# Kernel optimization log

Hardware: AMD Instinct MI355X
Metric: run time of the kernel (lower is better)

The kernel has to match this reference:

```python
import jax, jax.numpy as jnp
import numpy as np

B, S, D, H = 1, 2048, 4096, 32
HD = D // H  # 128


def setup_inputs() -> dict:
    key = jax.random.key(0)
    ks = jax.random.split(key, 6)
    x = jax.random.normal(ks[0], (B, S, D), dtype=jnp.float32)
    # rotary angles: standard llama freqs, position * inv_freq
    inv_freq = 1.0 / (10000.0 ** (jnp.arange(0, HD, 2, dtype=jnp.float32) / HD))  # (HD/2,)
    freqs = jnp.arange(S, dtype=jnp.float32)[:, None] * inv_freq[None, :]  # (S, HD/2)
    scale = 0.02
    wq = jax.random.normal(ks[1], (D, D), dtype=jnp.float32) * scale
    wk = jax.random.normal(ks[2], (D, D), dtype=jnp.float32) * scale
    wv = jax.random.normal(ks[3], (D, D), dtype=jnp.float32) * scale
    wo = jax.random.normal(ks[4], (D, D), dtype=jnp.float32) * scale
    return {"x": x, "freqs": freqs, "wq": wq, "wk": wk, "wv": wv, "wo": wo}


def _rope(t, cos, sin):
    # t: (B,S,H,HD); pairs are interleaved (complex view of last dim)
    b, s, h, d = t.shape
    t2 = t.reshape(b, s, h, d // 2, 2)
    t0, t1 = t2[..., 0], t2[..., 1]
    o0 = t0 * cos - t1 * sin
    o1 = t0 * sin + t1 * cos
    return jnp.stack([o0, o1], axis=-1).reshape(b, s, h, d)


def reference(x, freqs, wq, wk, wv, wo):
    b, s, d = x.shape
    hd = 2 * freqs.shape[-1]
    h = d // hd
    # projections (torch Linear: y = x @ W.T)
    q = (x @ wq.T).reshape(b, s, h, hd)
    k = (x @ wk.T).reshape(b, s, h, hd)
    v = (x @ wv.T).reshape(b, s, h, hd)
    cos = jnp.cos(freqs)[None, :s, None, :]  # (1,S,1,HD/2)
    sin = jnp.sin(freqs)[None, :s, None, :]
    q = _rope(q, cos, sin)
    k = _rope(k, cos, sin)
    q = q.transpose(0, 2, 1, 3)  # (B,H,S,HD)
    k = k.transpose(0, 2, 1, 3)
    v = v.transpose(0, 2, 1, 3)
    scale = jnp.sqrt(jnp.float32(hd))
    scores = jnp.einsum('bhqd,bhkd->bhqk', q, k).astype(jnp.float32) / scale
    # causal mask (qp == ep path): -inf strictly above diagonal
    mask = jnp.triu(jnp.full((s, s), -jnp.inf, dtype=scores.dtype), k=1)
    scores = scores + mask[None, None]
    attn = jax.nn.softmax(scores, axis=-1).astype(q.dtype)
    out = jnp.einsum('bhqk,bhkd->bhqd', attn, v)
    out = out.transpose(0, 2, 1, 3).reshape(b, s, d)
    return out @ wo.T
```

## Files before the change

kernel.cpp:

```cpp
#include <hip/hip_runtime.h>
#include <hip/hip_bf16.h>
#include <stdint.h>


typedef __attribute__((ext_vector_type(8))) short bf16x8;
typedef __attribute__((ext_vector_type(4))) float f32x4;

#define S_LEN 2048
#define DMODEL 4096
#define NHEAD 32
#define HDIM 128
#define QKV_LD 12288

#define QSCALE 0.1275247584969759f

__device__ __forceinline__ unsigned short f2bf(float f) {
  unsigned int u = __float_as_uint(f);
  unsigned int r = u + 0x7FFFu + ((u >> 16) & 1u);
  return (unsigned short)(r >> 16);
}
__device__ __forceinline__ float bf2f(unsigned short h) {
  return __uint_as_float(((unsigned int)h) << 16);
}
__device__ __forceinline__ void gl_lds16(const void* g, void* l) {
  __builtin_amdgcn_global_load_lds((const __attribute__((address_space(1))) unsigned int*)g,
                                   (__attribute__((address_space(3))) unsigned int*)l, 16, 0, 0);
}
__device__ __forceinline__ void phase_barrier() {
  __builtin_amdgcn_sched_barrier(0);
  asm volatile("" ::: "memory");
  __builtin_amdgcn_s_barrier();
  asm volatile("" ::: "memory");
  __builtin_amdgcn_sched_barrier(0);
}
__device__ __forceinline__ void wait_vmcnt6() {
  __builtin_amdgcn_sched_barrier(0);
  asm volatile("s_waitcnt vmcnt(6)" ::: "memory");
  __builtin_amdgcn_sched_barrier(0);
}
__device__ __forceinline__ void wait_vmcnt4() {
  __builtin_amdgcn_sched_barrier(0);
  asm volatile("s_waitcnt vmcnt(4)" ::: "memory");
  __builtin_amdgcn_sched_barrier(0);
}

__device__ __forceinline__ void cvt4(const float* __restrict__ s, unsigned short* __restrict__ d,
                                     int i) {
  float4 v = ((const float4*)s)[i];
  ushort4 o;
  o.x = f2bf(v.x); o.y = f2bf(v.y); o.z = f2bf(v.z); o.w = f2bf(v.w);
  ((ushort4*)d)[i] = o;
}

__global__ __launch_bounds__(256) void prep_inputs(const float* __restrict__ x,
                                                   const float* __restrict__ wq,
                                                   const float* __restrict__ wk,
                                                   const float* __restrict__ wv,
                                                   const float* __restrict__ fr,
                                                   unsigned short* __restrict__ xb,
                                                   unsigned short* __restrict__ wqkvb,
                                                   float* __restrict__ cs) {
  const int NX = 2097152;
  const int NW = 4194304;
  const int NR = S_LEN * 64;
  const int total = NX + 3 * NW + NR;
  int i = blockIdx.x * blockDim.x + threadIdx.x;
  int stride = gridDim.x * blockDim.x;
  for (; i < total; i += stride) {
    if (i < NX) {
      cvt4(x, xb, i);
    } else if (i < NX + NW) {
      cvt4(wq, wqkvb, i - NX);
    } else if (i < NX + 2 * NW) {
      cvt4(wk, wqkvb + 16777216, i - NX - NW);
    } else if (i < NX + 3 * NW) {
      cvt4(wv, wqkvb + 33554432, i - NX - 2 * NW);
    } else {
      int j = i - (NX + 3 * NW);
      float f = fr[j];
      cs[2 * j]     = cosf(f);
      cs[2 * j + 1] = sinf(f);
    }
  }
}

__device__ __forceinline__ void mfma_quad(f32x4 (&acc)[8][4], const bf16x8 (&af)[4][2],
                                          const bf16x8 (&bf)[2][2], int moff, int noff) {
  __builtin_amdgcn_s_setprio(1);
#pragma unroll
  for (int mi = 0; mi < 4; ++mi)
#pragma unroll
    for (int ni = 0; ni < 2; ++ni)
#pragma unroll
      for (int kk = 0; kk < 2; ++kk)
        acc[moff + mi][noff + ni] = __builtin_amdgcn_mfma_f32_16x16x32_bf16(
            af[mi][kk], bf[ni][kk], acc[moff + mi][noff + ni], 0, 0, 0);
  __builtin_amdgcn_s_setprio(0);
}
__device__ __forceinline__ void mfma_quad2(f32x4 (&acc)[4][4], const bf16x8 (&af)[2][2],
                                           const bf16x8 (&bf)[2][2], int moff, int noff) {
  __builtin_amdgcn_s_setprio(1);
#pragma unroll
  for (int mi = 0; mi < 2; ++mi)
#pragma unroll
    for (int ni = 0; ni < 2; ++ni)
#pragma unroll
      for (int kk = 0; kk < 2; ++kk)
        acc[moff + mi][noff + ni] = __builtin_amdgcn_mfma_f32_16x16x32_bf16(
            af[mi][kk], bf[ni][kk], acc[moff + mi][noff + ni], 0, 0, 0);
  __builtin_amdgcn_s_setprio(0);
}

__device__ __forceinline__ void read_a(bf16x8 (&dst)[4][2], const char* base, int half,
                                       int wr, int l15, int l4, int swz) {
#pragma unroll
  for (int mi = 0; mi < 4; ++mi) {
    const char* rb = base + (wr * 128 + half * 64 + mi * 16 + l15) * 128;
#pragma unroll
    for (int kk = 0; kk < 2; ++kk)
      dst[mi][kk] = *(const bf16x8*)(rb + ((kk * 64 + l4 * 16) ^ swz));
  }
}
__device__ __forceinline__ void read_b(bf16x8 (&dst)[2][2], const char* base, int half,
                                       int wc, int l15, int l4, int swz) {
#pragma unroll
  for (int ni = 0; ni < 2; ++ni) {
    const char* rb = base + (wc * 64 + half * 32 + ni * 16 + l15) * 128;
#pragma unroll
    for (int kk = 0; kk < 2; ++kk)
      dst[ni][kk] = *(const bf16x8*)(rb + ((kk * 64 + l4 * 16) ^ swz));
  }
}
__device__ __forceinline__ void read_a2(bf16x8 (&dst)[2][2], const char* base, int half,
                                        int wr, int l15, int l4, int swz) {
#pragma unroll
  for (int mi = 0; mi < 2; ++mi) {
    const char* rb = base + (wr * 64 + half * 32 + mi * 16 + l15) * 128;
#pragma unroll
    for (int kk = 0; kk < 2; ++kk)
      dst[mi][kk] = *(const bf16x8*)(rb + ((kk * 64 + l4 * 16) ^ swz));
  }
}
__device__ __forceinline__ void read_b2(bf16x8 (&dst)[2][2], const char* base, int half,
                                        int wc, int l15, int l4, int swz) {
#pragma unroll
  for (int ni = 0; ni < 2; ++ni) {
    const char* rb = base + (wc * 64 + half * 32 + ni * 16 + l15) * 128;
#pragma unroll
    for (int kk = 0; kk < 2; ++kk)
      dst[ni][kk] = *(const bf16x8*)(rb + ((kk * 64 + l4 * 16) ^ swz));
  }
}

template <bool OUT_BF16, bool ROPE>
__device__ __forceinline__ void gemm256_body(const unsigned short* __restrict__ A,
                                             const unsigned short* __restrict__ B,
                                             void* __restrict__ C,
                                             int M, int N, int K, int ldc,
                                             char* smem, int wg,
                                             const float* __restrict__ cs) {
  const int tid = threadIdx.x;
  const int lane = tid & 63, wid = tid >> 6;
  const int wr = wid >> 2, wc = wid & 3;
  const int l15 = lane & 15, l4 = lane >> 4;

  const int nbn = N >> 8;
  const int bm = wg / nbn, bn = wg % nbn;
  const int nk = K >> 6;

  unsigned short* AlB = (unsigned short*)smem;
  unsigned short* BlB = (unsigned short*)smem + 32768;

  const int srow = tid >> 3;
  const int scol = ((tid & 7) ^ (srow & 7)) * 8;
  const unsigned short* Asrc = A + (size_t)(bm * 256 + srow) * K + scol;
  const unsigned short* Bsrc = B + (size_t)(bn * 256 + srow) * K + scol;
  const int ldsdst = wid * 512;

#define STA(b, kt, q) gl_lds16(Asrc + ((size_t)(q) * 64) * K + (kt) * 64, AlB + (b) * 16384 + (q) * 4096 + ldsdst)
#define STB(b, kt, q) gl_lds16(Bsrc + ((size_t)(q) * 64) * K + (kt) * 64, BlB + (b) * 16384 + (q) * 4096 + ldsdst)

  const int swz = (l15 & 7) << 4;

  f32x4 acc[8][4] = {};
  bf16x8 Ax[4][2], Ay[4][2], B0f[2][2], B1f[2][2];

#pragma unroll
  for (int q = 0; q < 4; ++q) STA(0, 0, q);
#pragma unroll
  for (int q = 0; q < 4; ++q) STB(0, 0, q);
  {
    const int k1 = (nk > 1) ? 1 : 0;
    STA(1, k1, 0); STA(1, k1, 2);
    STB(1, k1, 0); STB(1, k1, 1); STB(1, k1, 2); STB(1, k1, 3);
  }
  wait_vmcnt6();
  phase_barrier();
  read_a(Ax, (const char*)AlB, 0, wr, l15, l4, swz);
  read_b(B0f, (const char*)BlB, 0, wc, l15, l4, swz);

#define HALF(bb, AC, AA, t)                                                \
  {                                                                        \
    const int kt1 = ((t) + 1 < nk) ? (t) + 1 : nk - 1;                     \
    const int kt2 = ((t) + 2 < nk) ? (t) + 2 : nk - 1;                     \
    const char* Ab = (const char*)(AlB + (bb) * 16384);                    \
    const char* Bb = (const char*)(BlB + (bb) * 16384);                    \
    const char* Abn = (const char*)(AlB + ((bb) ^ 1) * 16384);             \
    const char* Bbn = (const char*)(BlB + ((bb) ^ 1) * 16384);             \
    STA((bb) ^ 1, kt1, 1); STA((bb) ^ 1, kt1, 3);                          \
    phase_barrier();                                                       \
    mfma_quad(acc, AC, B0f, 0, 0);                                 \
    read_a(AA, Ab, 1, wr, l15, l4, swz);                                   \
    STA(bb, kt2, 0); STA(bb, kt2, 2);                                      \
    phase_barrier();                                                       \
    mfma_quad(acc, AA, B0f, 4, 0);                                 \
    read_b(B1f, Bb, 1, wc, l15, l4, swz);                                  \
    STB(bb, kt2, 0); STB(bb, kt2, 1);                                      \
    phase_barrier();                                                       \
    mfma_quad(acc, AA, B1f, 4, 2);                                 \
    STB(bb, kt2, 2); STB(bb, kt2, 3);                                      \
    wait_vmcnt6();                                                         \
    phase_barrier();                                                       \
    mfma_quad(acc, AC, B1f, 0, 2);                                 \
    read_a(AA, Abn, 0, wr, l15, l4, swz);                                  \
    read_b(B0f, Bbn, 0, wc, l15, l4, swz);                                 \
  }

  for (int t = 0; t < nk; t += 2) {
    HALF(0, Ax, Ay, t);
    HALF(1, Ay, Ax, t + 1);
  }
#undef HALF
#undef STA
#undef STB

  __builtin_amdgcn_sched_barrier(0);
  asm volatile("s_waitcnt vmcnt(0)" ::: "memory");

  const size_t crow0 = (size_t)bm * 256 + wr * 128 + l4 * 4;
  const int ccol0 = bn * 256 + wc * 64 + l15;
#pragma unroll
  for (int mf = 0; mf < 8; ++mf)
#pragma unroll
    for (int nf = 0; nf < 4; ++nf) {
      size_t row = crow0 + mf * 16;
      int col = ccol0 + nf * 16;
      if (ROPE) {
        const int d = col & (HDIM - 1);
        const int i2 = d & ~1;
        const float fs = (col < 4096) ? QSCALE : 1.0f;
        unsigned short* Cp = (unsigned short*)C;
#pragma unroll
        for (int r = 0; r < 4; ++r) {
          float v = acc[mf][nf][r];
          float vp = __shfl_xor(v, 1, 64);
          float2 csv = *(const float2*)&cs[(row + r) * HDIM + i2];
          float o = ((d & 1) == 0) ? (v * csv.x - vp * csv.y)
                                   : (vp * csv.y + v * csv.x);
          Cp[(row + r) * ldc + col] = f2bf(o * fs);
        }
      } else if (OUT_BF16) {
        unsigned short* Cp = (unsigned short*)C;
#pragma unroll
        for (int r = 0; r < 4; ++r) Cp[(row + r) * ldc + col] = f2bf(acc[mf][nf][r]);
      } else {
        float* Cp = (float*)C;
#pragma unroll
        for (int r = 0; r < 4; ++r) Cp[(row + r) * ldc + col] = acc[mf][nf][r];
      }
    }
}

template <bool OUT_BF16, bool VT_OUT>
__device__ __forceinline__ void gemm128_body(const unsigned short* __restrict__ A,
                                             const unsigned short* __restrict__ B,
                                             void* __restrict__ C,
                                             int M, int N, int K, int ldc,
                                             char* smem, int wg) {
  const int tid = threadIdx.x;
  const int lane = tid & 63, wid = tid >> 6;
  const int wr = wid >> 2, wc = wid & 3;
  const int l15 = lane & 15, l4 = lane >> 4;

  const int nbn = N >> 8;
  const int bm = wg / nbn, bn = wg % nbn;
  const int nk = K >> 6;

  unsigned short* AlB = (unsigned short*)smem;
  unsigned short* BlB = (unsigned short*)smem + 16384;

  const int srow = tid >> 3;
  const int scol = ((tid & 7) ^ (srow & 7)) * 8;
  const unsigned short* Asrc = A + (size_t)(bm * 128 + srow) * K + scol;
  const unsigned short* Bsrc = B + (size_t)(bn * 256 + srow) * K + scol;
  const int ldsdst = wid * 512;

#define STA2(b, kt, q) gl_lds16(Asrc + ((size_t)(q) * 64) * K + (kt) * 64, AlB + (b) * 8192 + (q) * 4096 + ldsdst)
#define STB2(b, kt, q) gl_lds16(Bsrc + ((size_t)(q) * 64) * K + (kt) * 64, BlB + (b) * 16384 + (q) * 4096 + ldsdst)

  const int swz = (l15 & 7) << 4;

  f32x4 acc[4][4] = {};
  bf16x8 Ax[2][2], Ay[2][2], B0f[2][2], B1f[2][2];

  STA2(0, 0, 0); STA2(0, 0, 1);
#pragma unroll
  for (int q = 0; q < 4; ++q) STB2(0, 0, q);
  {
    const int k1 = (nk > 1) ? 1 : 0;
    STA2(1, k1, 0); STA2(1, k1, 1);
    STB2(1, k1, 0); STB2(1, k1, 1);
  }
  wait_vmcnt4();
  phase_barrier();
  read_a2(Ax, (const char*)AlB, 0, wr, l15, l4, swz);
  read_b2(B0f, (const char*)BlB, 0, wc, l15, l4, swz);

#define HALF2(bb, AC, AA, t)                                               \
  {                                                                        \
    const int kt1 = ((t) + 1 < nk) ? (t) + 1 : nk - 1;                     \
    const int kt2 = ((t) + 2 < nk) ? (t) + 2 : nk - 1;                     \
    const char* Ab = (const char*)(AlB + (bb) * 8192);                     \
    const char* Bb = (const char*)(BlB + (bb) * 16384);                    \
    const char* Abn = (const char*)(AlB + ((bb) ^ 1) * 8192);              \
    const char* Bbn = (const char*)(BlB + ((bb) ^ 1) * 16384);             \
    STB2((bb) ^ 1, kt1, 2); STB2((bb) ^ 1, kt1, 3);        \
    phase_barrier();                                                       \
    mfma_quad2(acc, AC, B0f, 0, 0);                                \
    read_a2(AA, Ab, 1, wr, l15, l4, swz);                                  \
    STA2(bb, kt2, 0); STA2(bb, kt2, 1);                                    \
    phase_barrier();                                                       \
    mfma_quad2(acc, AA, B0f, 2, 0);                                \
    read_b2(B1f, Bb, 1, wc, l15, l4, swz);                                 \
    STB2(bb, kt2, 0); STB2(bb, kt2, 1);                                    \
    phase_barrier();                                                       \
    mfma_quad2(acc, AA, B1f, 2, 2);                                \
    wait_vmcnt4();                                                         \
    phase_barrier();                                                       \
    mfma_quad2(acc, AC, B1f, 0, 2);                                \
    read_a2(AA, Abn, 0, wr, l15, l4, swz);                                 \
    read_b2(B0f, Bbn, 0, wc, l15, l4, swz);                                \
  }

  for (int t = 0; t < nk; t += 2) {
    HALF2(0, Ax, Ay, t);
    HALF2(1, Ay, Ax, t + 1);
  }
#undef HALF2
#undef STA2
#undef STB2

  __builtin_amdgcn_sched_barrier(0);
  asm volatile("s_waitcnt vmcnt(0)" ::: "memory");

  if (VT_OUT) {
    unsigned short* Tw = (unsigned short*)smem + (size_t)wid * 4672;
#pragma unroll
    for (int mf = 0; mf < 4; ++mf)
#pragma unroll
      for (int nf = 0; nf < 4; ++nf)
#pragma unroll
        for (int r = 0; r < 4; ++r) {
          int lr = mf * 16 + l4 * 4 + r;
          int lc = nf * 16 + l15;
          Tw[lr * 73 + lc] = f2bf(acc[mf][nf][r]);
        }
    __syncthreads();
    unsigned short* vtp = (unsigned short*)C;
    const int gcol0 = bn * 256 + wc * 64;
    const int grow0 = bm * 128 + wr * 64;
    const int dl8 = lane >> 3, sc = lane & 7;
#pragma unroll
    for (int it = 0; it < 8; ++it) {
      int dl = it * 8 + dl8;
      unsigned short tmp[8];
#pragma unroll
      for (int j = 0; j < 8; ++j) tmp[j] = Tw[(sc * 8 + j) * 73 + dl];
      unsigned short* dst = vtp + (size_t)(gcol0 + dl) * S_LEN + grow0 + sc * 8;
      *(ushort4*)dst = make_ushort4(tmp[0], tmp[1], tmp[2], tmp[3]);
      *(ushort4*)(dst + 4) = make_ushort4(tmp[4], tmp[5], tmp[6], tmp[7]);
    }
    return;
  }

  const size_t crow0 = (size_t)bm * 128 + wr * 64 + l4 * 4;
  const int ccol0 = bn * 256 + wc * 64 + l15;
#pragma unroll
  for (int mf = 0; mf < 4; ++mf)
#pragma unroll
    for (int nf = 0; nf < 4; ++nf) {
      size_t row = crow0 + mf * 16;
      int col = ccol0 + nf * 16;
      if (OUT_BF16) {
        unsigned short* Cp = (unsigned short*)C;
#pragma unroll
        for (int r = 0; r < 4; ++r) Cp[(row + r) * ldc + col] = f2bf(acc[mf][nf][r]);
      } else {
        float* Cp = (float*)C;
#pragma unroll
        for (int r = 0; r < 4; ++r) Cp[(row + r) * ldc + col] = acc[mf][nf][r];
      }
    }
}

__global__ __launch_bounds__(512, 2) void qkv_proj(const unsigned short* __restrict__ xb,
                                                   const unsigned short* __restrict__ wqkvb,
                                                   unsigned short* __restrict__ qkvb,
                                                   unsigned short* __restrict__ vt,
                                                   const float* __restrict__ cs) {
  __shared__ __align__(16) char smem[131072];
  const int b = blockIdx.x;
  if (b < 256) {
    gemm256_body<true, true>(xb, wqkvb, qkvb, 2048, 8192, 4096, QKV_LD, smem, b, cs);
  } else {
    gemm128_body<true, true>(xb, wqkvb + 33554432, vt, 2048, 4096, 4096, 0, smem, b - 256);
  }
}

__global__ __launch_bounds__(512, 2) void out_proj(const unsigned short* __restrict__ A,
                                                   const unsigned short* __restrict__ B,
                                                   float* __restrict__ C) {
  __shared__ __align__(16) char smem[98304];
  gemm128_body<false, false>(A, B, C, 2048, 4096, 4096, 4096, smem, blockIdx.x);
}

__global__ __launch_bounds__(256) void attn_kernel(const unsigned short* __restrict__ qkv,
                                                   const unsigned short* __restrict__ vt,
                                                   float* __restrict__ pacc,
                                                   float* __restrict__ pm,
                                                   float* __restrict__ pl,
                                                   unsigned short* __restrict__ out,
                                                   const float* __restrict__ wo,
                                                   unsigned short* __restrict__ wob) {
  __shared__ __align__(16) unsigned short Klds[64 * 128];
  __shared__ __align__(16) unsigned short Vtlds[128 * 64];
  __shared__ __align__(16) unsigned short Plds[4][16 * 64];
  const int tid = threadIdx.x, lane = tid & 63, w = tid >> 6;
  const int l15 = lane & 15, l4 = lane >> 4;
  const int h = blockIdx.x & 31;
  const int jj = blockIdx.x >> 5;

  {
    const int NT = 1536 * 256;
    for (int i = blockIdx.x * 256 + tid; i < 4194304; i += NT) cvt4(wo, wob, i);
  }

  int bq, c, kt0, kt1;
  if (jj < 17) {
    bq = 31 - jj; c = 0; kt0 = 0; kt1 = 16;
  } else {
    int k = jj - 17;
    if (k == 0)      { bq = 31;            c = 1; }
    else if (k & 1)  { bq = 30 - (k >> 1); c = 1; }
    else             { bq = 15 - (k >> 1); c = 0; }
    kt0 = c ? 16 : 0;
    kt1 = bq + 1;
  }
  if (jj == 16) kt1 = 16;
  const int qw = bq * 64 + w * 16;

  bf16x8 qf[4];
#pragma unroll
  for (int ds = 0; ds < 4; ++ds)
    qf[ds] = *(const bf16x8*)&qkv[(size_t)(qw + l15) * QKV_LD + h * HDIM + ds * 32 + l4 * 8];

  f32x4 acc[8] = {};
  float m_run[4], l_run[4];
#pragma unroll
  for (int r = 0; r < 4; ++r) { m_run[r] = -1e30f; l_run[r] = 0.f; }

  for (int kt = kt0; kt < kt1; ++kt) {
    const int kv0 = kt * 64;
    __syncthreads();
#pragma unroll
    for (int i = 0; i < 4; ++i) {
      int b = (w * 4 + i) * 64 + lane;
      int r = b >> 4, cc = b & 15;
      gl_lds16(qkv + (size_t)(kv0 + r) * QKV_LD + 4096 + h * HDIM + ((cc ^ (r & 15)) * 8),
               &Klds[(w * 4 + i) * 512]);
    }
#pragma unroll
    for (int i = 0; i < 4; ++i) {
      int b = (w * 4 + i) * 64 + lane;
      int r = b >> 3, cc = b & 7;
      gl_lds16(vt + (size_t)(h * HDIM + r) * S_LEN + kv0 + ((cc ^ (r & 7)) * 8),
               &Vtlds[(w * 4 + i) * 512]);
    }
    __syncthreads();

    f32x4 s[4] = {};
    __builtin_amdgcn_s_setprio(1);
#pragma unroll
    for (int jt = 0; jt < 4; ++jt) {
      int kr = jt * 16 + l15;
#pragma unroll
      for (int ds = 0; ds < 4; ++ds) {
        int cc = (ds * 4 + l4) ^ (kr & 15);
        bf16x8 kf = *(const bf16x8*)&Klds[kr * 128 + cc * 8];
        s[jt] = __builtin_amdgcn_mfma_f32_16x16x32_bf16(qf[ds], kf, s[jt], 0, 0, 0);
      }
    }
    __builtin_amdgcn_s_setprio(0);

    const bool diag = (kt == bq);
    if (diag) {
#pragma unroll
      for (int jt = 0; jt < 4; ++jt)
#pragma unroll
        for (int r = 0; r < 4; ++r) {
          int kvg = kv0 + jt * 16 + l15;
          int qg = qw + l4 * 4 + r;
          if (kvg > qg) s[jt][r] = -1e30f;
        }
    }

    float alpha[4];
#pragma unroll
    for (int r = 0; r < 4; ++r) {
      float mx = fmaxf(fmaxf(s[0][r], s[1][r]), fmaxf(s[2][r], s[3][r]));
#pragma unroll
      for (int off = 1; off < 16; off <<= 1) mx = fmaxf(mx, __shfl_xor(mx, off, 64));
      float mi = fmaxf(m_run[r], mx);
      alpha[r] = exp2f(m_run[r] - mi);
      m_run[r] = mi;
      float sum = 0.f;
#pragma unroll
      for (int jt = 0; jt < 4; ++jt) {
        float p = exp2f(s[jt][r] - mi);
        s[jt][r] = p;
        sum += p;
      }
#pragma unroll
      for (int off = 1; off < 16; off <<= 1) sum += __shfl_xor(sum, off, 64);
      l_run[r] = l_run[r] * alpha[r] + sum;
    }
#pragma unroll
    for (int dt = 0; dt < 8; ++dt)
#pragma unroll
      for (int r = 0; r < 4; ++r) acc[dt][r] *= alpha[r];

    unsigned short* P = &Plds[w][0];
#pragma unroll
    for (int jt = 0; jt < 4; ++jt)
#pragma unroll
      for (int r = 0; r < 4; ++r) {
        int row = l4 * 4 + r, col = jt * 16 + l15;
        P[(row * 64 + col) ^ ((row & 7) << 3)] = f2bf(s[jt][r]);
      }

    __builtin_amdgcn_s_setprio(1);
#pragma unroll
    for (int ks = 0; ks < 2; ++ks) {
      bf16x8 pa = *(const bf16x8*)&P[(l15 * 64 + ks * 32 + l4 * 8) ^ ((l15 & 7) << 3)];
#pragma unroll
      for (int dt = 0; dt < 8; ++dt) {
        int vr = dt * 16 + l15;
        int cc = (ks * 4 + l4) ^ (vr & 7);
        bf16x8 vf = *(const bf16x8*)&Vtlds[vr * 64 + cc * 8];
        acc[dt] = __builtin_amdgcn_mfma_f32_16x16x32_bf16(pa, vf, acc[dt], 0, 0, 0);
      }
    }
    __builtin_amdgcn_s_setprio(0);
  }

  if (bq < 16) {
    float inv[4];
#pragma unroll
    for (int r = 0; r < 4; ++r) inv[r] = 1.f / l_run[r];
#pragma unroll
    for (int dt = 0; dt < 8; ++dt)
#pragma unroll
      for (int r = 0; r < 4; ++r) {
        int row = qw + l4 * 4 + r;
        int col = h * HDIM + dt * 16 + l15;
        out[(size_t)row * DMODEL + col] = f2bf(acc[dt][r] * inv[r]);
      }
  } else {
    const size_t bj = ((size_t)h * 32 + bq) * 2 + c;
    float* pa = pacc + bj * 8192 + (size_t)(w * 16) * 128;
#pragma unroll
    for (int dt = 0; dt < 8; ++dt)
#pragma unroll
      for (int r = 0; r < 4; ++r)
        pa[(l4 * 4 + r) * 128 + dt * 16 + l15] = acc[dt][r];
    if (l15 == 0) {
#pragma unroll
      for (int r = 0; r < 4; ++r) {
        pm[bj * 64 + w * 16 + l4 * 4 + r] = m_run[r];
        pl[bj * 64 + w * 16 + l4 * 4 + r] = l_run[r];
      }
    }
  }
}

__global__ __launch_bounds__(256) void attn_combine(const float* __restrict__ pacc,
                                                    const float* __restrict__ pm,
                                                    const float* __restrict__ pl,
                                                    unsigned short* __restrict__ out) {
  const int x = blockIdx.x;
  const int bq = 16 + (x >> 5), h = x & 31;
  const int tid = threadIdx.x;
  const int row = tid >> 2;
  const int d0 = (tid & 3) * 32;
  const size_t base = ((size_t)h * 32 + bq) * 2;
  const float m0 = pm[base * 64 + row];
  const float l0 = pl[base * 64 + row];
  float m1 = pm[(base + 1) * 64 + row];
  float l1 = pl[(base + 1) * 64 + row];
  float M = fmaxf(m0, m1);
  float w0 = exp2f(m0 - M);
  float w1 = exp2f(m1 - M);
  float denom = w0 * l0 + w1 * l1;
  const float inv = 1.f / denom;
  const float* a0 = pacc + base * 8192 + row * 128 + d0;
  const float* a1 = a0 + 8192;
  unsigned short* op = out + (size_t)(bq * 64 + row) * DMODEL + h * HDIM + d0;
#pragma unroll
  for (int i = 0; i < 8; ++i) {
    float4 v = *(const float4*)(a0 + i * 4);
    float4 u = *(const float4*)(a1 + i * 4);
    ushort4 o;
    o.x = f2bf((w0 * v.x + w1 * u.x) * inv);
    o.y = f2bf((w0 * v.y + w1 * u.y) * inv);
    o.z = f2bf((w0 * v.z + w1 * u.z) * inv);
    o.w = f2bf((w0 * v.w + w1 * u.w) * inv);
    *(ushort4*)(op + i * 4) = o;
  }
}

extern "C" void kernel_launch(void* const* d_in, const int* in_sizes, int n_in,
                              void* d_out, int out_size, void* d_ws, size_t ws_size,
                              hipStream_t stream) {
  const float* x = (const float*)d_in[0];
  const float* fr = (const float*)d_in[1];
  const float* wq = (const float*)d_in[2];
  const float* wk = (const float*)d_in[3];
  const float* wv = (const float*)d_in[4];
  const float* wo = (const float*)d_in[5];

  char* ws = (char*)d_ws;
  const size_t OFF_XB   = 0;
  const size_t OFF_WQKV = 16777216;
  const size_t OFF_WO   = OFF_WQKV + 100663296;
  const size_t OFF_QKV  = OFF_WO + 33554432;
  const size_t OFF_CS   = OFF_QKV + 50331648;
  const size_t OFF_VT   = OFF_CS + 1048576;
  const size_t OFF_ATTN = OFF_VT + 16777216;

  unsigned short* xb    = (unsigned short*)(ws + OFF_XB);
  unsigned short* wqkvb = (unsigned short*)(ws + OFF_WQKV);
  unsigned short* wob   = (unsigned short*)(ws + OFF_WO);
  unsigned short* qkvb  = (unsigned short*)(ws + OFF_QKV);
  float*          cs    = (float*)(ws + OFF_CS);
  unsigned short* vt    = (unsigned short*)(ws + OFF_VT);
  unsigned short* attn  = (unsigned short*)(ws + OFF_ATTN);
  float* pacc = (float*)(ws + OFF_WQKV);
  float* pm   = (float*)(ws + OFF_WQKV + 67108864);
  float* pl   = (float*)(ws + OFF_WQKV + 67633152);

  prep_inputs<<<2048, 256, 0, stream>>>(x, wq, wk, wv, fr, xb, wqkvb, cs);
  qkv_proj<<<dim3(512), 512, 0, stream>>>(xb, wqkvb, qkvb, vt, cs);
  attn_kernel<<<dim3(1536), 256, 0, stream>>>(qkvb, vt, pacc, pm, pl, attn, wo, wob);
  attn_combine<<<dim3(512), 256, 0, stream>>>(pacc, pm, pl, attn);
  out_proj<<<dim3(256), 512, 0, stream>>>(attn, wob, (float*)d_out);
}
```

Measured before the change: 406.9 us.

## Fuse split-KV attention combine into attn kernel via atomic arrival counter

Removes the separate attn_combine launch. Each split block writes its partial accumulator and its m/l statistics, then bumps a per-pair atomic counter. The second block to arrive reads its partner's partials and writes the merged, normalized bf16 output. Counters are zeroed by an extra block appended to qkv_proj, and the partial buffers are compacted to cover only the split rows. This saves one kernel launch and one pass over the partial data, at the cost of fences, atomics and an extra global read on the last-arriving block.

```diff
diff --git a/kernel.cpp b/kernel.cpp
--- a/kernel.cpp
+++ b/kernel.cpp
@@ -407,9 +407,14 @@
                                                    const unsigned short* __restrict__ wqkvb,
                                                    unsigned short* __restrict__ qkvb,
                                                    unsigned short* __restrict__ vt,
-                                                   const float* __restrict__ cs) {
+                                                   const float* __restrict__ cs,
+                                                   unsigned int* __restrict__ ctr) {
   __shared__ __align__(16) char smem[131072];
   const int b = blockIdx.x;
+  if (b == 512) {
+    if (threadIdx.x < 512) ctr[threadIdx.x] = 0;
+    return;
+  }
   if (b < 256) {
     gemm256_body<true, true>(xb, wqkvb, qkvb, 2048, 8192, 4096, QKV_LD, smem, b, cs);
   } else {
@@ -431,10 +436,12 @@
                                                    float* __restrict__ pl,
                                                    unsigned short* __restrict__ out,
                                                    const float* __restrict__ wo,
-                                                   unsigned short* __restrict__ wob) {
+                                                   unsigned short* __restrict__ wob,
+                                                   unsigned int* __restrict__ ctr) {
   __shared__ __align__(16) unsigned short Klds[64 * 128];
   __shared__ __align__(16) unsigned short Vtlds[128 * 64];
   __shared__ __align__(16) unsigned short Plds[4][16 * 64];
+  __shared__ unsigned int s_arrival;
   const int tid = threadIdx.x, lane = tid & 63, w = tid >> 6;
   const int l15 = lane & 15, l4 = lane >> 4;
   const int h = blockIdx.x & 31;
@@ -576,8 +583,9 @@
         out[(size_t)row * DMODEL + col] = f2bf(acc[dt][r] * inv[r]);
       }
   } else {
-    const size_t bj = ((size_t)h * 32 + bq) * 2 + c;
-    float* pa = pacc + bj * 8192 + (size_t)(w * 16) * 128;
+    const int pair = h * 16 + (bq - 16);
+    const size_t pj = (size_t)pair * 2 + c;
+    float* pa = pacc + pj * 8192 + (size_t)(w * 16) * 128;
 #pragma unroll
     for (int dt = 0; dt < 8; ++dt)
 #pragma unroll
@@ -586,45 +594,43 @@
     if (l15 == 0) {
 #pragma unroll
       for (int r = 0; r < 4; ++r) {
-        pm[bj * 64 + w * 16 + l4 * 4 + r] = m_run[r];
-        pl[bj * 64 + w * 16 + l4 * 4 + r] = l_run[r];
-      }
-    }
-  }
-}
-
-__global__ __launch_bounds__(256) void attn_combine(const float* __restrict__ pacc,
-                                                    const float* __restrict__ pm,
-                                                    const float* __restrict__ pl,
-                                                    unsigned short* __restrict__ out) {
-  const int x = blockIdx.x;
-  const int bq = 16 + (x >> 5), h = x & 31;
-  const int tid = threadIdx.x;
-  const int row = tid >> 2;
-  const int d0 = (tid & 3) * 32;
-  const size_t base = ((size_t)h * 32 + bq) * 2;
-  const float m0 = pm[base * 64 + row];
-  const float l0 = pl[base * 64 + row];
-  float m1 = pm[(base + 1) * 64 + row];
-  float l1 = pl[(base + 1) * 64 + row];
-  float M = fmaxf(m0, m1);
-  float w0 = exp2f(m0 - M);
-  float w1 = exp2f(m1 - M);
-  float denom = w0 * l0 + w1 * l1;
-  const float inv = 1.f / denom;
-  const float* a0 = pacc + base * 8192 + row * 128 + d0;
-  const float* a1 = a0 + 8192;
-  unsigned short* op = out + (size_t)(bq * 64 + row) * DMODEL + h * HDIM + d0;
-#pragma unroll
-  for (int i = 0; i < 8; ++i) {
-    float4 v = *(const float4*)(a0 + i * 4);
-    float4 u = *(const float4*)(a1 + i * 4);
-    ushort4 o;
-    o.x = f2bf((w0 * v.x + w1 * u.x) * inv);
-    o.y = f2bf((w0 * v.y + w1 * u.y) * inv);
-    o.z = f2bf((w0 * v.z + w1 * u.z) * inv);
-    o.w = f2bf((w0 * v.w + w1 * u.w) * inv);
-    *(ushort4*)(op + i * 4) = o;
+        pm[pj * 64 + w * 16 + l4 * 4 + r] = m_run[r];
+        pl[pj * 64 + w * 16 + l4 * 4 + r] = l_run[r];
+      }
+    }
+    __threadfence();
+    if (tid == 0) s_arrival = atomicAdd(&ctr[pair], 1u);
+    __syncthreads();
+    if (s_arrival & 1u) {
+      __threadfence();
+      const size_t po = pj ^ 1;
+      const float* om = pm + po * 64;
+      const float* ol = pl + po * 64;
+      const float* oa = pacc + po * 8192;
+      float wS[4], wO[4], inv[4];
+#pragma unroll
+      for (int r = 0; r < 4; ++r) {
+        int row = w * 16 + l4 * 4 + r;
+        float mo = om[row];
+        float lo = ol[row];
+        float M = fmaxf(m_run[r], mo);
+        wS[r] = exp2f(m_run[r] - M);
+        wO[r] = exp2f(mo - M);
+        inv[r] = 1.f / (wS[r] * l_run[r] + wO[r] * lo);
+      }
+#pragma unroll
+      for (int dt = 0; dt < 8; ++dt)
+#pragma unroll
+        for (int r = 0; r < 4; ++r) {
+          int lrow = w * 16 + l4 * 4 + r;
+          int lcol = dt * 16 + l15;
+          float ov = oa[lrow * 128 + lcol];
+          int row = qw + l4 * 4 + r;
+          int col = h * HDIM + lcol;
+          out[(size_t)row * DMODEL + col] =
+              f2bf((wS[r] * acc[dt][r] + wO[r] * ov) * inv[r]);
+        }
+    }
   }
 }
 
@@ -655,12 +661,12 @@
   unsigned short* vt    = (unsigned short*)(ws + OFF_VT);
   unsigned short* attn  = (unsigned short*)(ws + OFF_ATTN);
   float* pacc = (float*)(ws + OFF_WQKV);
-  float* pm   = (float*)(ws + OFF_WQKV + 67108864);
-  float* pl   = (float*)(ws + OFF_WQKV + 67633152);
+  float* pm   = (float*)(ws + OFF_WQKV + 33554432);
+  float* pl   = (float*)(ws + OFF_WQKV + 33816576);
+  unsigned int* ctr = (unsigned int*)(ws + OFF_WQKV + 34078720);
 
   prep_inputs<<<2048, 256, 0, stream>>>(x, wq, wk, wv, fr, xb, wqkvb, cs);
-  qkv_proj<<<dim3(512), 512, 0, stream>>>(xb, wqkvb, qkvb, vt, cs);
-  attn_kernel<<<dim3(1536), 256, 0, stream>>>(qkvb, vt, pacc, pm, pl, attn, wo, wob);
-  attn_combine<<<dim3(512), 256, 0, stream>>>(pacc, pm, pl, attn);
+  qkv_proj<<<dim3(513), 512, 0, stream>>>(xb, wqkvb, qkvb, vt, cs, ctr);
+  attn_kernel<<<dim3(1536), 256, 0, stream>>>(qkvb, vt, pacc, pm, pl, attn, wo, wob, ctr);
   out_proj<<<dim3(256), 512, 0, stream>>>(attn, wob, (float*)d_out);
 }
```

New measurement: 621.4 us. +52.7%, slower.
